# Kernel optimization log

Measured on AMD Instinct MI355X. Metric: run time of the kernel, lower is better.

The kernel has to match this reference:

```python
import jax, jax.numpy as jnp
import numpy as np
from jax import lax


def setup_inputs() -> dict:
    key = jax.random.key(0)
    ks = jax.random.split(key, 6)
    B = 65536
    x = jax.random.normal(ks[0], (B, 784), dtype=jnp.float32)
    conv_w = jax.random.normal(ks[1], (3, 3), dtype=jnp.float32)
    w1 = jax.random.normal(ks[2], (676, 128), dtype=jnp.float32) * 0.05
    b1 = jax.random.normal(ks[3], (128,), dtype=jnp.float32) * 0.05
    w2 = jax.random.normal(ks[4], (128, 10), dtype=jnp.float32) * 0.05
    b2 = jax.random.normal(ks[5], (10,), dtype=jnp.float32) * 0.05
    return {"x": x, "conv_w": conv_w, "w1": w1, "b1": b1, "w2": w2, "b2": b2}


def reference(x, conv_w, w1, b1, w2, b2):
    B = x.shape[0]
    img = x.reshape(B, 1, 28, 28)  # NCHW
    # valid 3x3 cross-correlation (tensordot over patch == cross-correlation)
    conv = lax.conv_general_dilated(
        img, conv_w[None, None], window_strides=(1, 1), padding="VALID",
        dimension_numbers=("NCHW", "OIHW", "NCHW"))  # [B,1,26,26]
    h = conv.reshape(B, 26 * 26)
    h = jax.nn.relu(h @ w1 + b1)
    return h @ w2 + b2
```

## Files before the change

### kernel.cpp

```cpp
#include <hip/hip_runtime.h>

typedef __attribute__((ext_vector_type(4))) float floatx4;
typedef __attribute__((ext_vector_type(8))) short short8;
typedef __attribute__((ext_vector_type(8))) unsigned short ushort8v;

__device__ __forceinline__ unsigned short f2bf(float f) {
  unsigned int u = __builtin_bit_cast(unsigned int, f);
  u += 0x7FFFu + ((u >> 16) & 1u);
  return (unsigned short)(u >> 16);
}

#define KTOT 784
#define KP   800
#define N1   128
#define BM   128
#define BK   32
#define LDH  132

__global__ void prep_w1eff(const float* __restrict__ conv_w,
                           const float* __restrict__ w1,
                           unsigned short* __restrict__ Bt) {
  const int n = blockIdx.x;
  float cw[9];
#pragma unroll
  for (int i = 0; i < 9; ++i) cw[i] = conv_w[i];
  for (int q = threadIdx.x; q < KP; q += blockDim.x) {
    float acc = 0.f;
    if (q < KTOT) {
      const int r = q / 28, c = q % 28;
#pragma unroll
      for (int di = 0; di < 3; ++di) {
        const int i2 = r - di;
        if (i2 < 0 || i2 >= 26) continue;
#pragma unroll
        for (int dj = 0; dj < 3; ++dj) {
          const int j2 = c - dj;
          if (j2 < 0 || j2 >= 26) continue;
          acc += cw[di * 3 + dj] * w1[(i2 * 26 + j2) * N1 + n];
        }
      }
    }
    Bt[n * KP + q] = f2bf(acc);
  }
}

__global__ __launch_bounds__(256, 2)
void fused_mlp(const float* __restrict__ x,
               const unsigned short* __restrict__ Bt,
               const float* __restrict__ b1,
               const float* __restrict__ w2,
               const float* __restrict__ b2,
               float* __restrict__ out) {
  __shared__ __align__(16) unsigned short sH[BM * LDH];
  __shared__ __align__(16) unsigned short sW2t[16 * LDH];
  __shared__ float sB1[N1];
  __shared__ float sB2[16];

  const int tid  = threadIdx.x;
  const int wave = tid >> 6;
  const int lane = tid & 63;
  const int wm = wave & 1;
  const int wn = wave >> 1;
  const int lr = lane & 15;
  const int lq = lane >> 4;

  const long row_base = (long)blockIdx.x * BM;
  const float* xblk = x + row_base * KTOT;

  for (int i = tid; i < 16 * N1; i += 256) {
    const int n = i >> 7, k = i & 127;
    sW2t[n * LDH + k] = (n < 10) ? f2bf(w2[k * 10 + n]) : (unsigned short)0;
  }
  if (tid < N1) sB1[tid] = b1[tid];
  if (tid < 10) sB2[tid] = b2[tid];

  const float* arow[4];
  const unsigned short* brow[4];
#pragma unroll
  for (int i = 0; i < 4; ++i)
    arow[i] = xblk + (long)(wm * 64 + i * 16 + lr) * KTOT;
#pragma unroll
  for (int j = 0; j < 4; ++j)
    brow[j] = Bt + (long)(wn * 64 + j * 16 + lr) * KP + lq * 8;

  floatx4 acc[4][4] = {};

  auto load_a = [&](floatx4 (&ra)[4][2], int kt) {
    int kk = kt * BK + lq * 8;
    if (kk >= KTOT) kk = 0;
#pragma unroll
    for (int i = 0; i < 4; ++i) {
      ra[i][0] = *(const floatx4*)(arow[i] + kk);
      ra[i][1] = *(const floatx4*)(arow[i] + kk + 4);
    }
  };
  auto load_b = [&](ushort8v (&rb)[4], int kt) {
    const int k0 = kt * BK;
#pragma unroll
    for (int j = 0; j < 4; ++j)
      rb[j] = *(const ushort8v*)(brow[j] + k0);
  };
  auto compute = [&](const floatx4 (&ra)[4][2], const ushort8v (&rb)[4]) {
    short8 af[4];
#pragma unroll
    for (int i = 0; i < 4; ++i) {
      ushort8v u;
      u[0] = f2bf(ra[i][0][0]); u[1] = f2bf(ra[i][0][1]);
      u[2] = f2bf(ra[i][0][2]); u[3] = f2bf(ra[i][0][3]);
      u[4] = f2bf(ra[i][1][0]); u[5] = f2bf(ra[i][1][1]);
      u[6] = f2bf(ra[i][1][2]); u[7] = f2bf(ra[i][1][3]);
      af[i] = __builtin_bit_cast(short8, u);
    }
#pragma unroll
    for (int im = 0; im < 4; ++im)
#pragma unroll
      for (int in = 0; in < 4; ++in)
        acc[im][in] = __builtin_amdgcn_mfma_f32_16x16x32_bf16(
            af[im], __builtin_bit_cast(short8, rb[in]), acc[im][in], 0, 0, 0);
  };

  floatx4 ra0[4][2], ra1[4][2];
  ushort8v rb0[4], rb1[4];
  load_a(ra0, 0);
  load_b(rb0, 0);
  for (int kt = 0; kt < 24; kt += 2) {
    load_a(ra1, kt + 1);
    load_b(rb1, kt + 1);
    compute(ra0, rb0);
    load_a(ra0, kt + 2);
    load_b(rb0, kt + 2);
    compute(ra1, rb1);
  }
  compute(ra0, rb0);

  __syncthreads();

#pragma unroll
  for (int im = 0; im < 4; ++im) {
#pragma unroll
    for (int in = 0; in < 4; ++in) {
      const int col = wn * 64 + in * 16 + lr;
      const float bb = sB1[col];
#pragma unroll
      for (int r = 0; r < 4; ++r) {
        const int row = wm * 64 + im * 16 + lq * 4 + r;
        const float v = acc[im][in][r] + bb;
        sH[row * LDH + col] = f2bf(v > 0.f ? v : 0.f);
      }
    }
  }
  __syncthreads();

  floatx4 o0 = {0.f, 0.f, 0.f, 0.f}, o1 = {0.f, 0.f, 0.f, 0.f};
  const int m0 = wave * 32;
#pragma unroll
  for (int kc = 0; kc < 4; ++kc) {
    const int kof = kc * 32 + lq * 8;
    const short8 wv = *(const short8*)&sW2t[lr * LDH + kof];
    const short8 a0 = *(const short8*)&sH[(m0 + lr) * LDH + kof];
    const short8 a1 = *(const short8*)&sH[(m0 + 16 + lr) * LDH + kof];
    o0 = __builtin_amdgcn_mfma_f32_16x16x32_bf16(a0, wv, o0, 0, 0, 0);
    o1 = __builtin_amdgcn_mfma_f32_16x16x32_bf16(a1, wv, o1, 0, 0, 0);
  }
  if (lr < 10) {
    const float bb = sB2[lr];
#pragma unroll
    for (int r = 0; r < 4; ++r) {
      const long row = row_base + m0 + lq * 4 + r;
      out[row * 10 + lr] = o0[r] + bb;
      out[(row + 16) * 10 + lr] = o1[r] + bb;
    }
  }
}

extern "C" void kernel_launch(void* const* d_in, const int* in_sizes, int n_in,
                              void* d_out, int out_size, void* d_ws, size_t ws_size,
                              hipStream_t stream) {
  const float* x      = (const float*)d_in[0];
  const float* conv_w = (const float*)d_in[1];
  const float* w1     = (const float*)d_in[2];
  const float* b1     = (const float*)d_in[3];
  const float* w2     = (const float*)d_in[4];
  const float* b2     = (const float*)d_in[5];
  float* out = (float*)d_out;

  unsigned short* Bt = (unsigned short*)d_ws;

  prep_w1eff<<<128, 256, 0, stream>>>(conv_w, w1, Bt);
  fused_mlp<<<65536 / BM, 256, 0, stream>>>(x, Bt, b1, w2, b2, out);
}
```

Before: 335.1 us.

## Stage bf16 input rows in LDS with coalesced two-phase loads, shrink block to 32 rows

Each block now covers 32 rows instead of 128. The block loads its whole fp32 input tile with coalesced float4 loads in two chunks, converts it to bf16 once and stores it in shared memory. The second chunk is loaded while the first chunk's MFMAs run. Each wave computes a 32x32 output slice, reading its A fragments from LDS and its B fragments from global memory with double buffering. This replaces the strided per-lane global reads of x with contiguous streaming, at the cost of much more LDS per block (about 51KB) and more redundant reads of the weight matrix across blocks.

```diff
diff --git a/kernel.cpp b/kernel.cpp
--- a/kernel.cpp
+++ b/kernel.cpp
@@ -2,6 +2,7 @@
 
 typedef __attribute__((ext_vector_type(4))) float floatx4;
 typedef __attribute__((ext_vector_type(8))) short short8;
+typedef __attribute__((ext_vector_type(4))) unsigned short ushort4v;
 typedef __attribute__((ext_vector_type(8))) unsigned short ushort8v;
 
 __device__ __forceinline__ unsigned short f2bf(float f) {
@@ -13,9 +14,13 @@
 #define KTOT 784
 #define KP   800
 #define N1   128
-#define BM   128
-#define BK   32
+#define BM   32
+#define LDK  804
 #define LDH  132
+#define CK0  104
+#define CK1  96
+
+#define LBAR() do { __builtin_amdgcn_s_waitcnt(0xC07F); __builtin_amdgcn_s_barrier(); } while (0)
 
 __global__ void prep_w1eff(const float* __restrict__ conv_w,
                            const float* __restrict__ w1,
@@ -51,6 +56,7 @@
                const float* __restrict__ w2,
                const float* __restrict__ b2,
                float* __restrict__ out) {
+  __shared__ __align__(16) unsigned short sAk[BM * LDK];
   __shared__ __align__(16) unsigned short sH[BM * LDH];
   __shared__ __align__(16) unsigned short sW2t[16 * LDH];
   __shared__ float sB1[N1];
@@ -59,13 +65,20 @@
   const int tid  = threadIdx.x;
   const int wave = tid >> 6;
   const int lane = tid & 63;
-  const int wm = wave & 1;
-  const int wn = wave >> 1;
+  const int wn = wave;
   const int lr = lane & 15;
   const int lq = lane >> 4;
 
   const long row_base = (long)blockIdx.x * BM;
   const float* xblk = x + row_base * KTOT;
+
+  floatx4 v0[13];
+#pragma unroll
+  for (int i = 0; i < 13; ++i) {
+    const int idx = tid + 256 * i;
+    const int r = idx / CK0, ks = idx % CK0;
+    v0[i] = *(const floatx4*)(xblk + (long)r * KTOT + ks * 4);
+  }
 
   for (int i = tid; i < 16 * N1; i += 256) {
     const int n = i >> 7, k = i & 127;
@@ -74,101 +87,109 @@
   if (tid < N1) sB1[tid] = b1[tid];
   if (tid < 10) sB2[tid] = b2[tid];
 
-  const float* arow[4];
-  const unsigned short* brow[4];
-#pragma unroll
-  for (int i = 0; i < 4; ++i)
-    arow[i] = xblk + (long)(wm * 64 + i * 16 + lr) * KTOT;
-#pragma unroll
-  for (int j = 0; j < 4; ++j)
-    brow[j] = Bt + (long)(wn * 64 + j * 16 + lr) * KP + lq * 8;
-
-  floatx4 acc[4][4] = {};
-
-  auto load_a = [&](floatx4 (&ra)[4][2], int kt) {
-    int kk = kt * BK + lq * 8;
-    if (kk >= KTOT) kk = 0;
-#pragma unroll
-    for (int i = 0; i < 4; ++i) {
-      ra[i][0] = *(const floatx4*)(arow[i] + kk);
-      ra[i][1] = *(const floatx4*)(arow[i] + kk + 4);
-    }
+#pragma unroll
+  for (int i = 0; i < 13; ++i) {
+    const int idx = tid + 256 * i;
+    const int r = idx / CK0, ks = idx % CK0;
+    ushort4v u;
+    u[0] = f2bf(v0[i][0]); u[1] = f2bf(v0[i][1]);
+    u[2] = f2bf(v0[i][2]); u[3] = f2bf(v0[i][3]);
+    *(ushort4v*)&sAk[r * LDK + ks * 4] = u;
+  }
+
+  const unsigned short* btb = Bt + (long)(wn * 32 + lr) * KP + lq * 8;
+  ushort8v bb0[2], bb1[2];
+  auto loadB = [&](ushort8v* d, int kt) {
+    d[0] = *(const ushort8v*)(btb + kt * 32);
+    d[1] = *(const ushort8v*)(btb + 16 * KP + kt * 32);
   };
-  auto load_b = [&](ushort8v (&rb)[4], int kt) {
-    const int k0 = kt * BK;
-#pragma unroll
-    for (int j = 0; j < 4; ++j)
-      rb[j] = *(const ushort8v*)(brow[j] + k0);
+  loadB(bb0, 0);
+  loadB(bb1, 1);
+
+  floatx4 v1[12];
+#pragma unroll
+  for (int i = 0; i < 12; ++i) {
+    const int idx = tid + 256 * i;
+    const int r = idx / CK1;
+    int k = (CK0 + idx % CK1) * 4;
+    if (k > KTOT - 4) k = KTOT - 4;
+    v1[i] = *(const floatx4*)(xblk + (long)r * KTOT + k);
+  }
+
+  LBAR();
+
+  floatx4 acc[2][2] = {};
+  auto mstep = [&](int kt, const ushort8v* b) {
+    short8 af[2];
+#pragma unroll
+    for (int i = 0; i < 2; ++i)
+      af[i] = *(const short8*)&sAk[(i * 16 + lr) * LDK + kt * 32 + lq * 8];
+#pragma unroll
+    for (int im = 0; im < 2; ++im)
+#pragma unroll
+      for (int in = 0; in < 2; ++in)
+        acc[im][in] = __builtin_amdgcn_mfma_f32_16x16x32_bf16(
+            af[im], __builtin_bit_cast(short8, b[in]), acc[im][in], 0, 0, 0);
   };
-  auto compute = [&](const floatx4 (&ra)[4][2], const ushort8v (&rb)[4]) {
-    short8 af[4];
-#pragma unroll
-    for (int i = 0; i < 4; ++i) {
-      ushort8v u;
-      u[0] = f2bf(ra[i][0][0]); u[1] = f2bf(ra[i][0][1]);
-      u[2] = f2bf(ra[i][0][2]); u[3] = f2bf(ra[i][0][3]);
-      u[4] = f2bf(ra[i][1][0]); u[5] = f2bf(ra[i][1][1]);
-      u[6] = f2bf(ra[i][1][2]); u[7] = f2bf(ra[i][1][3]);
-      af[i] = __builtin_bit_cast(short8, u);
-    }
-#pragma unroll
-    for (int im = 0; im < 4; ++im)
-#pragma unroll
-      for (int in = 0; in < 4; ++in)
-        acc[im][in] = __builtin_amdgcn_mfma_f32_16x16x32_bf16(
-            af[im], __builtin_bit_cast(short8, rb[in]), acc[im][in], 0, 0, 0);
-  };
-
-  floatx4 ra0[4][2], ra1[4][2];
-  ushort8v rb0[4], rb1[4];
-  load_a(ra0, 0);
-  load_b(rb0, 0);
-  for (int kt = 0; kt < 24; kt += 2) {
-    load_a(ra1, kt + 1);
-    load_b(rb1, kt + 1);
-    compute(ra0, rb0);
-    load_a(ra0, kt + 2);
-    load_b(rb0, kt + 2);
-    compute(ra1, rb1);
-  }
-  compute(ra0, rb0);
-
-  __syncthreads();
-
-#pragma unroll
-  for (int im = 0; im < 4; ++im) {
-#pragma unroll
-    for (int in = 0; in < 4; ++in) {
-      const int col = wn * 64 + in * 16 + lr;
-      const float bb = sB1[col];
+
+#pragma unroll
+  for (int kt = 0; kt <= 12; ++kt) {
+    mstep(kt, (kt & 1) ? bb1 : bb0);
+    if (kt + 2 <= 12) loadB((kt & 1) ? bb1 : bb0, kt + 2);
+  }
+  loadB(bb1, 13);
+  loadB(bb0, 14);
+
+#pragma unroll
+  for (int i = 0; i < 12; ++i) {
+    const int idx = tid + 256 * i;
+    const int r = idx / CK1, ks = CK0 + idx % CK1;
+    ushort4v u;
+    u[0] = f2bf(v1[i][0]); u[1] = f2bf(v1[i][1]);
+    u[2] = f2bf(v1[i][2]); u[3] = f2bf(v1[i][3]);
+    *(ushort4v*)&sAk[r * LDK + ks * 4] = u;
+  }
+  LBAR();
+
+#pragma unroll
+  for (int kt = 13; kt <= 24; ++kt) {
+    mstep(kt, (kt & 1) ? bb1 : bb0);
+    if (kt + 2 <= 24) loadB((kt & 1) ? bb1 : bb0, kt + 2);
+  }
+
+#pragma unroll
+  for (int im = 0; im < 2; ++im) {
+#pragma unroll
+    for (int in = 0; in < 2; ++in) {
+      const int col = wn * 32 + in * 16 + lr;
+      const float bbv = sB1[col];
 #pragma unroll
       for (int r = 0; r < 4; ++r) {
-        const int row = wm * 64 + im * 16 + lq * 4 + r;
-        const float v = acc[im][in][r] + bb;
+        const int row = im * 16 + lq * 4 + r;
+        const float v = acc[im][in][r] + bbv;
         sH[row * LDH + col] = f2bf(v > 0.f ? v : 0.f);
       }
     }
   }
   __syncthreads();
 
-  floatx4 o0 = {0.f, 0.f, 0.f, 0.f}, o1 = {0.f, 0.f, 0.f, 0.f};
-  const int m0 = wave * 32;
-#pragma unroll
-  for (int kc = 0; kc < 4; ++kc) {
-    const int kof = kc * 32 + lq * 8;
-    const short8 wv = *(const short8*)&sW2t[lr * LDH + kof];
-    const short8 a0 = *(const short8*)&sH[(m0 + lr) * LDH + kof];
-    const short8 a1 = *(const short8*)&sH[(m0 + 16 + lr) * LDH + kof];
-    o0 = __builtin_amdgcn_mfma_f32_16x16x32_bf16(a0, wv, o0, 0, 0, 0);
-    o1 = __builtin_amdgcn_mfma_f32_16x16x32_bf16(a1, wv, o1, 0, 0, 0);
-  }
-  if (lr < 10) {
-    const float bb = sB2[lr];
-#pragma unroll
-    for (int r = 0; r < 4; ++r) {
-      const long row = row_base + m0 + lq * 4 + r;
-      out[row * 10 + lr] = o0[r] + bb;
-      out[(row + 16) * 10 + lr] = o1[r] + bb;
+  if (wave < 2) {
+    floatx4 o0 = {0.f, 0.f, 0.f, 0.f};
+    const int m0 = wave * 16;
+#pragma unroll
+    for (int kc = 0; kc < 4; ++kc) {
+      const int kof = kc * 32 + lq * 8;
+      const short8 wv = *(const short8*)&sW2t[lr * LDH + kof];
+      const short8 a0 = *(const short8*)&sH[(m0 + lr) * LDH + kof];
+      o0 = __builtin_amdgcn_mfma_f32_16x16x32_bf16(a0, wv, o0, 0, 0, 0);
+    }
+    if (lr < 10) {
+      const float bbv = sB2[lr];
+#pragma unroll
+      for (int r = 0; r < 4; ++r) {
+        const long row = row_base + m0 + lq * 4 + r;
+        out[row * 10 + lr] = o0[r] + bbv;
+      }
     }
   }
 }
```

Result: faster. 314.0 us (-6.3%).
